# Optimization experiments

Hardware: AMD Instinct MI355X
Metric: run time of the kernel (lower is better)

Reference implementation:

```python
import jax, jax.numpy as jnp
import numpy as np

B, H, P, L = 8, 128, 128, 4096


def _cplx(x):
    # view_as_complex: (..., 2) float -> complex
    return x[..., 0] + 1j * x[..., 1]


def setup_inputs() -> dict:
    key = jax.random.key(0)
    ks = jax.random.split(key, 6)
    u = jax.random.normal(ks[0], (B, H, L), dtype=jnp.float32)
    C_ri = jax.random.normal(ks[1], (H, P, 2), dtype=jnp.float32)
    D_ri = jax.random.normal(ks[2], (H, H, 2), dtype=jnp.float32)
    # ContinuousStateReservoir: Re(Lambda) in [high_stability, low_stability] = [-1.0, -0.1]
    lam_re = jax.random.uniform(ks[3], (P,), minval=-1.0, maxval=-0.1, dtype=jnp.float32)
    lam_im = jax.random.normal(ks[4], (P,), dtype=jnp.float32) * np.float32(np.pi)
    Lam = lam_re + 1j * lam_im                      # continuous eigs
    Lam_bar = jnp.exp(Lam)                          # ZOH with Delta = 1
    B0 = jax.random.normal(ks[5], (P, H, 2), dtype=jnp.float32)
    Bc = _cplx(B0)
    B_bar = ((Lam_bar - 1.0) / Lam)[:, None] * Bc   # ZOH B_bar
    B_ri = jnp.stack([B_bar.real, B_bar.imag], axis=-1).astype(jnp.float32)
    Lambda_ri = jnp.stack([Lam_bar.real, Lam_bar.imag], axis=-1).astype(jnp.float32)
    return {"u": u, "C_ri": C_ri, "D_ri": D_ri, "B_ri": B_ri, "Lambda_ri": Lambda_ri}


def reference(u, C_ri, D_ri, B_ri, Lambda_ri):
    C = _cplx(C_ri)          # (H, P) complex
    D = _cplx(D_ri)          # (H, H)
    B_bar = _cplx(B_ri)      # (P, H)
    Lam_bar = _cplx(Lambda_ri)  # (P,)
    # torch.fft.rfftn defaults to ALL dims: complex FFT on (B,H), real FFT on L
    U_s = jnp.fft.rfftn(u)                                   # (B, H, Lf)
    s = 1j * (2.0 * jnp.pi * jnp.fft.rfftfreq(u.shape[-1]))  # (Lf,)
    mid = 1.0 / (s[None, :] - Lam_bar[:, None])              # (P, Lf) Cauchy kernel
    C_mid = jnp.einsum('hp,pl->hpl', C, mid)                 # (H, P, Lf)
    G = jnp.einsum('hpl,pq->hql', C_mid, B_bar)              # (H, H, Lf) transfer function
    Y_s = jnp.einsum('hql,bql->bhl', G, U_s) + jnp.einsum('hq,bql->bhl', D, U_s)
    y = jnp.fft.irfftn(Y_s)                                  # (B, H, L) real
    return jax.nn.gelu(y, approximate=False)
```

## Files before the change

kernel.cpp:

```cpp
#include <hip/hip_runtime.h>
#include <math.h>

#define Bn 8
#define Hn 128
#define Pn 128
#define Ln 4096
#define LF 2049
#define NROWS (Bn*Hn)
#define NT 32
#define NTILES 65
#define PLSZ 4096
#define WPLSZ 16384
#define TSCALE 64.0f

#define SKEW(a) ((a) + ((a) >> 4))
#define FBUF 2176

typedef _Float16 f16x8 __attribute__((ext_vector_type(8)));
typedef float f32x4 __attribute__((ext_vector_type(4)));

__device__ __forceinline__ void fsincos(float a, float* s, float* c) {
    *s = __sinf(a);
    *c = __cosf(a);
}

__device__ __forceinline__ void write2(_Float16* __restrict__ W, int idx,
                                       float vr, float vi) {
    W[0 * WPLSZ + idx] = (_Float16)vr;
    W[1 * WPLSZ + idx] = (_Float16)vi;
}

__global__ __launch_bounds__(256) void prep_all_k(
        const float* __restrict__ B_ri, const float* __restrict__ C_ri,
        const float* __restrict__ D_ri,
        _Float16* __restrict__ W1, _Float16* __restrict__ W2,
        _Float16* __restrict__ W3, float2* __restrict__ tw) {
    __shared__ float2 roots[128];
    __shared__ float2 stage[2048];
    __shared__ float2 Gs[8 * 128];
    const int bid = blockIdx.x;
    const int tid = threadIdx.x;

    if (tid < 128) {
        float ang = 3.14159265358979f * (float)tid / 64.0f;
        float sw, cw; fsincos(ang, &sw, &cw);
        roots[tid] = make_float2(cw, sw);
    }
    __syncthreads();

    if (bid < 64) {
        const float2* B2f = (const float2*)B_ri;
        stage[tid] = B2f[bid * 256 + tid];
        __syncthreads();
        const int pl = tid >> 7, h = tid & 127;
        float sr = 0.f, si = 0.f;
        #pragma unroll 8
        for (int q = 0; q < 128; ++q) {
            float2 rt = roots[(q * h) & 127];
            float2 bv = stage[(pl << 7) + q];
            sr += bv.x * rt.x + bv.y * rt.y;
            si += bv.y * rt.x - bv.x * rt.y;
        }
        write2(W1, bid * 256 + tid, sr, si);
    } else if (bid < 128) {
        const int bid2 = bid - 64;
        const float2* C2f = (const float2*)C_ri;
        const int h = 2 * bid2 + (tid >> 7), p = tid & 127;
        float sr = 0.f, si = 0.f;
        for (int chunk = 0; chunk < 8; ++chunk) {
            __syncthreads();
            #pragma unroll
            for (int i = 0; i < 8; ++i) stage[tid + i * 256] = C2f[chunk * 2048 + tid + i * 256];
            __syncthreads();
            #pragma unroll
            for (int j = 0; j < 16; ++j) {
                int h2 = chunk * 16 + j;
                float2 cv = stage[j * 128 + p];
                float2 rt = roots[(h * h2) & 127];
                sr += cv.x * rt.x - cv.y * rt.y;
                si += cv.x * rt.y + cv.y * rt.x;
            }
        }
        write2(W2, bid2 * 256 + tid, sr * (TSCALE / 128.0f), si * (TSCALE / 128.0f));
    } else if (bid < 144) {
        const int h0 = (bid - 128) * 8;
        const int hh = tid >> 5, ci = tid & 31;
        const float2* D2f = (const float2*)D_ri;
        float2 g[4];
        #pragma unroll
        for (int cc = 0; cc < 4; ++cc) g[cc] = make_float2(0.f, 0.f);
        for (int chunk = 0; chunk < 8; ++chunk) {
            __syncthreads();
            #pragma unroll
            for (int i = 0; i < 8; ++i) stage[tid + i * 256] = D2f[chunk * 2048 + tid + i * 256];
            __syncthreads();
            #pragma unroll
            for (int j = 0; j < 16; ++j) {
                int a = chunk * 16 + j;
                float2 rt = roots[((h0 + hh) * a) & 127];
                #pragma unroll
                for (int cc = 0; cc < 4; ++cc) {
                    float2 dv = stage[j * 128 + ci + 32 * cc];
                    g[cc].x += dv.x * rt.x - dv.y * rt.y;
                    g[cc].y += dv.x * rt.y + dv.y * rt.x;
                }
            }
        }
        #pragma unroll
        for (int cc = 0; cc < 4; ++cc)
            Gs[hh * 128 + ci + 32 * cc] = make_float2(g[cc].x * (1.0f / 128.0f),
                                                      g[cc].y * (1.0f / 128.0f));
        __syncthreads();
        float2 wacc[4];
        #pragma unroll
        for (int qq = 0; qq < 4; ++qq) wacc[qq] = make_float2(0.f, 0.f);
        #pragma unroll 4
        for (int c = 0; c < 128; ++c) {
            float2 gv = Gs[hh * 128 + c];
            #pragma unroll
            for (int qq = 0; qq < 4; ++qq) {
                int q = ci + 32 * qq;
                float2 rt = roots[(c * q) & 127];
                wacc[qq].x += gv.x * rt.x + gv.y * rt.y;
                wacc[qq].y += gv.y * rt.x - gv.x * rt.y;
            }
        }
        #pragma unroll
        for (int qq = 0; qq < 4; ++qq)
            write2(W3, (h0 + hh) * 128 + ci + 32 * qq, wacc[qq].x, wacc[qq].y);
    } else {
        int m = (bid - 144) * 256 + tid;
        float ang = -3.14159265358979f * (float)m / 1024.0f;
        float sw, cw;
        __sincosf(ang, &sw, &cw);
        tw[m] = make_float2(cw, sw);
    }
}

__device__ __forceinline__ float2 cadd2(float2 a, float2 b) { return make_float2(a.x + b.x, a.y + b.y); }
__device__ __forceinline__ float2 csub2(float2 a, float2 b) { return make_float2(a.x - b.x, a.y - b.y); }

template <int SIGN>
__device__ __forceinline__ void dft4(float2 a0, float2 a1, float2 a2, float2 a3,
                                     float2& y0, float2& y1, float2& y2, float2& y3) {
    float t0x = a0.x + a2.x, t0y = a0.y + a2.y;
    float t1x = a0.x - a2.x, t1y = a0.y - a2.y;
    float t2x = a1.x + a3.x, t2y = a1.y + a3.y;
    float t3x = a1.x - a3.x, t3y = a1.y - a3.y;
    y0 = make_float2(t0x + t2x, t0y + t2y);
    y2 = make_float2(t0x - t2x, t0y - t2y);
    y1 = make_float2(t1x - (float)SIGN * t3y, t1y + (float)SIGN * t3x);
    y3 = make_float2(t1x + (float)SIGN * t3y, t1y - (float)SIGN * t3x);
}

template <int SIGN>
__device__ __forceinline__ void fft2048(float2* bufA, float2* bufB,
                                        const float2* __restrict__ tw) {
    const int tid = threadIdx.x;
    float2* src = bufA;
    float2* dst = bufB;
    #pragma unroll
    for (int stg = 0; stg < 3; ++stg) {
        const int ls = 3 * stg;
        const int k = tid;
        const int q = k & ((1 << ls) - 1);
        const int mbase = k - q;
        float2 a[8];
        #pragma unroll
        for (int u = 0; u < 8; ++u) a[u] = src[SKEW(k + (u << 8))];
        float2 t1 = tw[mbase],     t2 = tw[2 * mbase], t3 = tw[3 * mbase];
        float2 t4 = tw[4 * mbase], t5 = tw[5 * mbase], t6 = tw[6 * mbase];
        float2 t7 = tw[7 * mbase];
        float2 A0, A1, A2, A3, B0, B1, B2, B3;
        dft4<SIGN>(a[0], a[2], a[4], a[6], A0, A1, A2, A3);
        dft4<SIGN>(a[1], a[3], a[5], a[7], B0, B1, B2, B3);
        const float c45 = 0.70710678118655f;
        float2 w1 = make_float2(c45 * (B1.x - (float)SIGN * B1.y), c45 * ((float)SIGN * B1.x + B1.y));
        float2 w2 = make_float2(-(float)SIGN * B2.y, (float)SIGN * B2.x);
        float2 w3 = make_float2(c45 * (-B3.x - (float)SIGN * B3.y), c45 * ((float)SIGN * B3.x - B3.y));
        float2 b[8];
        b[0] = cadd2(A0, B0);  b[4] = csub2(A0, B0);
        b[1] = cadd2(A1, w1);  b[5] = csub2(A1, w1);
        b[2] = cadd2(A2, w2);  b[6] = csub2(A2, w2);
        b[3] = cadd2(A3, w3);  b[7] = csub2(A3, w3);
        float2 twj[8];
        twj[1] = t1; twj[2] = t2; twj[3] = t3; twj[4] = t4;
        twj[5] = t5; twj[6] = t6; twj[7] = t7;
        #pragma unroll
        for (int j = 1; j < 8; ++j) {
            float cj = twj[j].x;
            float sj = (float)SIGN * twj[j].y;
            b[j] = make_float2(b[j].x * cj + b[j].y * sj, -b[j].x * sj + b[j].y * cj);
        }
        const int base = q + (mbase << 3);
        #pragma unroll
        for (int j = 0; j < 8; ++j) dst[SKEW(base + (j << ls))] = b[j];
        __syncthreads();
        float2* t = src; src = dst; dst = t;
    }
    #pragma unroll
    for (int r = 0; r < 2; ++r) {
        int k = tid + (r << 8);
        float2 a0 = src[SKEW(k)];
        float2 a1 = src[SKEW(k + 512)];
        float2 a2 = src[SKEW(k + 1024)];
        float2 a3 = src[SKEW(k + 1536)];
        float2 y0, y1, y2, y3;
        dft4<SIGN>(a0, a1, a2, a3, y0, y1, y2, y3);
        dst[SKEW(k)] = y0;
        dst[SKEW(k + 512)] = y1;
        dst[SKEW(k + 1024)] = y2;
        dst[SKEW(k + 1536)] = y3;
    }
    __syncthreads();
}

__global__ __launch_bounds__(256, 4) void rfft_rows_k(const float* __restrict__ u,
                                                      float2* __restrict__ Uhat,
                                                      const float2* __restrict__ tw) {
    __shared__ __align__(16) float2 bufA[FBUF];
    __shared__ __align__(16) float2 bufB[FBUF];
    const int row = blockIdx.x;
    const int tid = threadIdx.x;
    const float4* up4 = (const float4*)(u + (size_t)row * Ln);
    #pragma unroll
    for (int r = 0; r < 4; ++r) {
        float4 v = up4[tid + (r << 8)];
        int i = 2 * (tid + (r << 8));
        bufA[SKEW(i)] = make_float2(v.x, v.y);
        bufA[SKEW(i + 1)] = make_float2(v.z, v.w);
    }
    __syncthreads();
    fft2048<-1>(bufA, bufB, tw);
    float2* op = Uhat + (size_t)row * LF;
    for (int l = tid; l < 1025; l += 256) {
        float2 Zl = bufA[SKEW(l)];
        float2 Zm = bufA[SKEW((2048 - l) & 2047)];
        float2 Fe = make_float2(0.5f * (Zl.x + Zm.x), 0.5f * (Zl.y - Zm.y));
        float2 Dv = make_float2(0.5f * (Zl.x - Zm.x), 0.5f * (Zl.y + Zm.y));
        float2 Fo = make_float2(Dv.y, -Dv.x);
        float s, c; fsincos(-3.14159265358979f * (float)l / 2048.0f, &s, &c);
        float2 TF = make_float2(Fo.x * c - Fo.y * s, Fo.x * s + Fo.y * c);
        op[l] = make_float2(Fe.x + TF.x, Fe.y + TF.y);
        op[2048 - l] = make_float2(Fe.x - TF.x, -(Fe.y - TF.y));
    }
}

__global__ __launch_bounds__(256, 4) void irfft_gelu_k(const float2* __restrict__ Uhat,
                                                       float* __restrict__ out,
                                                       const float2* __restrict__ tw) {
    __shared__ __align__(16) float2 bufA[FBUF];
    __shared__ __align__(16) float2 bufB[FBUF];
    const int row = blockIdx.x;
    const int tid = threadIdx.x;
    const float2* wp = Uhat + (size_t)row * LF;
    for (int l = tid; l < 1025; l += 256) {
        float2 Ul = wp[l];
        float2 Um = wp[2048 - l];
        float2 Fe = make_float2(0.5f * (Ul.x + Um.x), 0.5f * (Ul.y - Um.y));
        float2 Dv = make_float2(0.5f * (Ul.x - Um.x), 0.5f * (Ul.y + Um.y));
        float s, c; fsincos(3.14159265358979f * (float)l / 2048.0f, &s, &c);
        float2 Fo = make_float2(Dv.x * c - Dv.y * s, Dv.x * s + Dv.y * c);
        bufA[SKEW(l)] = make_float2(Fe.x - Fo.y, Fe.y + Fo.x);
        if (l >= 1 && l <= 1023)
            bufA[SKEW(2048 - l)] = make_float2(Fe.x + Fo.y, Fo.x - Fe.y);
    }
    __syncthreads();
    fft2048<1>(bufA, bufB, tw);
    float4* op4 = (float4*)(out + (size_t)row * Ln);
    #pragma unroll
    for (int r = 0; r < 4; ++r) {
        int n = 2 * (tid + (r << 8));
        float2 z0 = bufA[SKEW(n)];
        float2 z1 = bufA[SKEW(n + 1)];
        float y0 = z0.x * (1.0f / 2048.0f);
        float y1 = z0.y * (1.0f / 2048.0f);
        float y2 = z1.x * (1.0f / 2048.0f);
        float y3 = z1.y * (1.0f / 2048.0f);
        op4[tid + (r << 8)] = make_float4(
            0.5f * y0 * (1.0f + erff(y0 * 0.70710678118655f)),
            0.5f * y1 * (1.0f + erff(y1 * 0.70710678118655f)),
            0.5f * y2 * (1.0f + erff(y2 * 0.70710678118655f)),
            0.5f * y3 * (1.0f + erff(y3 * 0.70710678118655f)));
    }
}

__device__ __forceinline__ f32x4 mfma16h(f16x8 a, f16x8 b, f32x4 c) {
    return __builtin_amdgcn_mfma_f32_16x16x32_f16(a, b, c, 0, 0, 0);
}
__device__ __forceinline__ f16x8 read_frag(const _Float16* plane, int n, int k) {
    int ksw = k ^ ((n & 7) << 3);
    return *(const f16x8*)(plane + n * 128 + ksw);
}
__device__ __forceinline__ f16x8 aread(const _Float16* W, int pl, int m, int k) {
    return *(const f16x8*)(W + pl * WPLSZ + m * 128 + k);
}

__global__ __launch_bounds__(256, 4) void mixmm_k(float2* __restrict__ Uhat,
                                                  const _Float16* __restrict__ W1,
                                                  const _Float16* __restrict__ W2,
                                                  const _Float16* __restrict__ W3,
                                                  const float* __restrict__ Lam) {
    __shared__ __align__(16) _Float16 Up[2 * PLSZ];
    __shared__ __align__(16) _Float16 Tp[2 * PLSZ];

    const int tid = threadIdx.x;
    const int b = blockIdx.x / NTILES;
    const int tile = blockIdx.x % NTILES;
    const int l0 = tile * NT;
    const int ncols = (LF - l0) < NT ? (LF - l0) : NT;

    {
        int n = tid & 31, kc = tid >> 5;
        float2 v[16];
        #pragma unroll
        for (int j = 0; j < 16; ++j) {
            int h = kc * 16 + j;
            v[j] = (n < ncols) ? Uhat[(size_t)(b * 128 + h) * LF + l0 + n]
                               : make_float2(0.f, 0.f);
        }
        #pragma unroll
        for (int jc = 0; jc < 2; ++jc) {
            f16x8 fr, fi;
            #pragma unroll
            for (int j = 0; j < 8; ++j) {
                fr[j] = (_Float16)v[jc * 8 + j].x;
                fi[j] = (_Float16)v[jc * 8 + j].y;
            }
            int ksw = (kc * 16 + jc * 8) ^ ((n & 7) << 3);
            *(f16x8*)(Up + 0 * PLSZ + n * 128 + ksw) = fr;
            *(f16x8*)(Up + 1 * PLSZ + n * 128 + ksw) = fi;
        }
    }
    __syncthreads();

    const int lane = tid & 63;
    const int w = tid >> 6;
    const int m15 = lane & 15;
    const int quad = lane >> 4;

    f32x4 accR[2][2], accM[2][2], accI[2][2];
    #pragma unroll
    for (int s = 0; s < 2; ++s)
        #pragma unroll
        for (int t = 0; t < 2; ++t) {
            accR[s][t] = (f32x4)0.f; accM[s][t] = (f32x4)0.f; accI[s][t] = (f32x4)0.f;
        }

    #pragma unroll
    for (int kb = 0; kb < 4; ++kb) {
        int k = kb * 32 + quad * 8;
        f16x8 wr[2], wi[2];
        #pragma unroll
        for (int s = 0; s < 2; ++s) {
            int m = w * 32 + s * 16 + m15;
            wr[s] = aread(W1, 0, m, k);
            wi[s] = aread(W1, 1, m, k);
        }
        f16x8 br[2], bi[2];
        #pragma unroll
        for (int t = 0; t < 2; ++t) {
            br[t] = read_frag(Up + 0 * PLSZ, t * 16 + m15, k);
            bi[t] = read_frag(Up + 1 * PLSZ, t * 16 + m15, k);
        }
        #pragma unroll
        for (int s = 0; s < 2; ++s)
            #pragma unroll
            for (int t = 0; t < 2; ++t) {
                accR[s][t] = mfma16h(wr[s], br[t], accR[s][t]);
                accM[s][t] = mfma16h(wi[s], bi[t], accM[s][t]);
                accI[s][t] = mfma16h(wr[s], bi[t], accI[s][t]);
                accI[s][t] = mfma16h(wi[s], br[t], accI[s][t]);
            }
    }

    #pragma unroll
    for (int s = 0; s < 2; ++s) {
        #pragma unroll
        for (int reg = 0; reg < 4; ++reg) {
            int p = w * 32 + s * 16 + quad * 4 + reg;
            float2 lamv = ((const float2*)Lam)[p];
            float dr = -lamv.x;
            #pragma unroll
            for (int t = 0; t < 2; ++t) {
                int n = t * 16 + m15;
                int l = l0 + n;
                float di = 3.14159265358979f * (float)l / 2048.0f - lamv.y;
                float inv = (1.0f / TSCALE) / (dr * dr + di * di);
                float xr = accR[s][t][reg] - accM[s][t][reg];
                float xi = accI[s][t][reg];
                float tr = (xr * dr + xi * di) * inv;
                float ti = (xi * dr - xr * di) * inv;
                int off = n * 128 + (p ^ ((n & 7) << 3));
                Tp[0 * PLSZ + off] = (_Float16)tr;
                Tp[1 * PLSZ + off] = (_Float16)ti;
            }
        }
    }
    __syncthreads();

    #pragma unroll
    for (int s = 0; s < 2; ++s)
        #pragma unroll
        for (int t = 0; t < 2; ++t) {
            accR[s][t] = (f32x4)0.f; accM[s][t] = (f32x4)0.f; accI[s][t] = (f32x4)0.f;
        }

    #pragma unroll
    for (int kb = 0; kb < 4; ++kb) {
        int k = kb * 32 + quad * 8;
        {
            f16x8 wr[2], wi[2];
            #pragma unroll
            for (int s = 0; s < 2; ++s) {
                int m = w * 32 + s * 16 + m15;
                wr[s] = aread(W2, 0, m, k);
                wi[s] = aread(W2, 1, m, k);
            }
            f16x8 br[2], bi[2];
            #pragma unroll
            for (int t = 0; t < 2; ++t) {
                br[t] = read_frag(Tp + 0 * PLSZ, t * 16 + m15, k);
                bi[t] = read_frag(Tp + 1 * PLSZ, t * 16 + m15, k);
            }
            #pragma unroll
            for (int s = 0; s < 2; ++s)
                #pragma unroll
                for (int t = 0; t < 2; ++t) {
                    accR[s][t] = mfma16h(wr[s], br[t], accR[s][t]);
                    accM[s][t] = mfma16h(wi[s], bi[t], accM[s][t]);
                    accI[s][t] = mfma16h(wr[s], bi[t], accI[s][t]);
                    accI[s][t] = mfma16h(wi[s], br[t], accI[s][t]);
                }
        }
        {
            f16x8 wr[2], wi[2];
            #pragma unroll
            for (int s = 0; s < 2; ++s) {
                int m = w * 32 + s * 16 + m15;
                wr[s] = aread(W3, 0, m, k);
                wi[s] = aread(W3, 1, m, k);
            }
            f16x8 br[2], bi[2];
            #pragma unroll
            for (int t = 0; t < 2; ++t) {
                br[t] = read_frag(Up + 0 * PLSZ, t * 16 + m15, k);
                bi[t] = read_frag(Up + 1 * PLSZ, t * 16 + m15, k);
            }
            #pragma unroll
            for (int s = 0; s < 2; ++s)
                #pragma unroll
                for (int t = 0; t < 2; ++t) {
                    accR[s][t] = mfma16h(wr[s], br[t], accR[s][t]);
                    accM[s][t] = mfma16h(wi[s], bi[t], accM[s][t]);
                    accI[s][t] = mfma16h(wr[s], bi[t], accI[s][t]);
                    accI[s][t] = mfma16h(wi[s], br[t], accI[s][t]);
                }
        }
    }

    #pragma unroll
    for (int s = 0; s < 2; ++s) {
        #pragma unroll
        for (int t = 0; t < 2; ++t) {
            int n = t * 16 + m15;
            if (n < ncols) {
                #pragma unroll
                for (int reg = 0; reg < 4; ++reg) {
                    int m = w * 32 + s * 16 + quad * 4 + reg;
                    Uhat[(size_t)(b * 128 + m) * LF + l0 + n] =
                        make_float2(accR[s][t][reg] - accM[s][t][reg], accI[s][t][reg]);
                }
            }
        }
    }
}

extern "C" void kernel_launch(void* const* d_in, const int* in_sizes, int n_in,
                              void* d_out, int out_size, void* d_ws, size_t ws_size,
                              hipStream_t stream) {
    const float* u    = (const float*)d_in[0];
    const float* C_ri = (const float*)d_in[1];
    const float* D_ri = (const float*)d_in[2];
    const float* B_ri = (const float*)d_in[3];
    const float* Lam  = (const float*)d_in[4];
    float* out = (float*)d_out;

    float2* Uhat = (float2*)d_ws;
    _Float16* W1 = (_Float16*)(Uhat + (size_t)NROWS * LF);
    _Float16* W2 = W1 + 2 * WPLSZ;
    _Float16* W3 = W2 + 2 * WPLSZ;
    float2* tw = (float2*)(W3 + 2 * WPLSZ);

    prep_all_k<<<152, 256, 0, stream>>>(B_ri, C_ri, D_ri, W1, W2, W3, tw);
    rfft_rows_k<<<NROWS, 256, 0, stream>>>(u, Uhat, tw);
    mixmm_k<<<Bn * NTILES, 256, 0, stream>>>(Uhat, W1, W2, W3, Lam);
    irfft_gelu_k<<<NROWS, 256, 0, stream>>>(Uhat, out, tw);
}
```

Measured before the change: 153.8 us.

## Replace radix-8 shared-memory FFT with four-step FFT using MFMA 128-point DFT

The 2048-point row FFTs in the forward and inverse kernels now use a 16x128 four-step decomposition. The radix-16 stage runs in registers, and the 128-point DFT stage runs as an fp16 MFMA matrix multiply against a precomputed DFT matrix. Each block now handles two rows, and the inverse FFT is done through conjugation. This moves FFT arithmetic onto the matrix cores and cuts the number of shared-memory passes and barriers. The cost is fp16 rounding of intermediate spectra, which adds accuracy risk, plus lower occupancy from launch bounds of 3 and larger shared memory.

```diff
diff --git a/kernel.cpp b/kernel.cpp
--- a/kernel.cpp
+++ b/kernel.cpp
@@ -3,7 +3,6 @@
 
 #define Bn 8
 #define Hn 128
-#define Pn 128
 #define Ln 4096
 #define LF 2049
 #define NROWS (Bn*Hn)
@@ -12,9 +11,12 @@
 #define PLSZ 4096
 #define WPLSZ 16384
 #define TSCALE 64.0f
+#define ISCALE 64.0f
 
 #define SKEW(a) ((a) + ((a) >> 4))
-#define FBUF 2176
+#define ZROW 2064
+#define XROW 2176
+#define ZIDX(n) (129 * ((n) >> 7) + ((n) & 127))
 
 typedef _Float16 f16x8 __attribute__((ext_vector_type(8)));
 typedef float f32x4 __attribute__((ext_vector_type(4)));
@@ -22,6 +24,22 @@
 __device__ __forceinline__ void fsincos(float a, float* s, float* c) {
     *s = __sinf(a);
     *c = __cosf(a);
+}
+__device__ __forceinline__ float2 cm(float2 a, float2 b) {
+    return make_float2(a.x * b.x - a.y * b.y, a.x * b.y + a.y * b.x);
+}
+
+template <int SIGN>
+__device__ __forceinline__ void dft4(float2 a0, float2 a1, float2 a2, float2 a3,
+                                     float2& y0, float2& y1, float2& y2, float2& y3) {
+    float t0x = a0.x + a2.x, t0y = a0.y + a2.y;
+    float t1x = a0.x - a2.x, t1y = a0.y - a2.y;
+    float t2x = a1.x + a3.x, t2y = a1.y + a3.y;
+    float t3x = a1.x - a3.x, t3y = a1.y - a3.y;
+    y0 = make_float2(t0x + t2x, t0y + t2y);
+    y2 = make_float2(t0x - t2x, t0y - t2y);
+    y1 = make_float2(t1x - (float)SIGN * t3y, t1y + (float)SIGN * t3x);
+    y3 = make_float2(t1x + (float)SIGN * t3y, t1y - (float)SIGN * t3x);
 }
 
 __device__ __forceinline__ void write2(_Float16* __restrict__ W, int idx,
@@ -34,7 +52,8 @@
         const float* __restrict__ B_ri, const float* __restrict__ C_ri,
         const float* __restrict__ D_ri,
         _Float16* __restrict__ W1, _Float16* __restrict__ W2,
-        _Float16* __restrict__ W3, float2* __restrict__ tw) {
+        _Float16* __restrict__ W3, float2* __restrict__ tw,
+        _Float16* __restrict__ F128) {
     __shared__ float2 roots[128];
     __shared__ float2 stage[2048];
     __shared__ float2 Gs[8 * 128];
@@ -128,160 +147,22 @@
         #pragma unroll
         for (int qq = 0; qq < 4; ++qq)
             write2(W3, (h0 + hh) * 128 + ci + 32 * qq, wacc[qq].x, wacc[qq].y);
-    } else {
+    } else if (bid < 152) {
         int m = (bid - 144) * 256 + tid;
         float ang = -3.14159265358979f * (float)m / 1024.0f;
         float sw, cw;
         __sincosf(ang, &sw, &cw);
         tw[m] = make_float2(cw, sw);
-    }
-}
-
-__device__ __forceinline__ float2 cadd2(float2 a, float2 b) { return make_float2(a.x + b.x, a.y + b.y); }
-__device__ __forceinline__ float2 csub2(float2 a, float2 b) { return make_float2(a.x - b.x, a.y - b.y); }
-
-template <int SIGN>
-__device__ __forceinline__ void dft4(float2 a0, float2 a1, float2 a2, float2 a3,
-                                     float2& y0, float2& y1, float2& y2, float2& y3) {
-    float t0x = a0.x + a2.x, t0y = a0.y + a2.y;
-    float t1x = a0.x - a2.x, t1y = a0.y - a2.y;
-    float t2x = a1.x + a3.x, t2y = a1.y + a3.y;
-    float t3x = a1.x - a3.x, t3y = a1.y - a3.y;
-    y0 = make_float2(t0x + t2x, t0y + t2y);
-    y2 = make_float2(t0x - t2x, t0y - t2y);
-    y1 = make_float2(t1x - (float)SIGN * t3y, t1y + (float)SIGN * t3x);
-    y3 = make_float2(t1x + (float)SIGN * t3y, t1y - (float)SIGN * t3x);
-}
-
-template <int SIGN>
-__device__ __forceinline__ void fft2048(float2* bufA, float2* bufB,
-                                        const float2* __restrict__ tw) {
-    const int tid = threadIdx.x;
-    float2* src = bufA;
-    float2* dst = bufB;
-    #pragma unroll
-    for (int stg = 0; stg < 3; ++stg) {
-        const int ls = 3 * stg;
-        const int k = tid;
-        const int q = k & ((1 << ls) - 1);
-        const int mbase = k - q;
-        float2 a[8];
-        #pragma unroll
-        for (int u = 0; u < 8; ++u) a[u] = src[SKEW(k + (u << 8))];
-        float2 t1 = tw[mbase],     t2 = tw[2 * mbase], t3 = tw[3 * mbase];
-        float2 t4 = tw[4 * mbase], t5 = tw[5 * mbase], t6 = tw[6 * mbase];
-        float2 t7 = tw[7 * mbase];
-        float2 A0, A1, A2, A3, B0, B1, B2, B3;
-        dft4<SIGN>(a[0], a[2], a[4], a[6], A0, A1, A2, A3);
-        dft4<SIGN>(a[1], a[3], a[5], a[7], B0, B1, B2, B3);
-        const float c45 = 0.70710678118655f;
-        float2 w1 = make_float2(c45 * (B1.x - (float)SIGN * B1.y), c45 * ((float)SIGN * B1.x + B1.y));
-        float2 w2 = make_float2(-(float)SIGN * B2.y, (float)SIGN * B2.x);
-        float2 w3 = make_float2(c45 * (-B3.x - (float)SIGN * B3.y), c45 * ((float)SIGN * B3.x - B3.y));
-        float2 b[8];
-        b[0] = cadd2(A0, B0);  b[4] = csub2(A0, B0);
-        b[1] = cadd2(A1, w1);  b[5] = csub2(A1, w1);
-        b[2] = cadd2(A2, w2);  b[6] = csub2(A2, w2);
-        b[3] = cadd2(A3, w3);  b[7] = csub2(A3, w3);
-        float2 twj[8];
-        twj[1] = t1; twj[2] = t2; twj[3] = t3; twj[4] = t4;
-        twj[5] = t5; twj[6] = t6; twj[7] = t7;
-        #pragma unroll
-        for (int j = 1; j < 8; ++j) {
-            float cj = twj[j].x;
-            float sj = (float)SIGN * twj[j].y;
-            b[j] = make_float2(b[j].x * cj + b[j].y * sj, -b[j].x * sj + b[j].y * cj);
-        }
-        const int base = q + (mbase << 3);
-        #pragma unroll
-        for (int j = 0; j < 8; ++j) dst[SKEW(base + (j << ls))] = b[j];
-        __syncthreads();
-        float2* t = src; src = dst; dst = t;
-    }
-    #pragma unroll
-    for (int r = 0; r < 2; ++r) {
-        int k = tid + (r << 8);
-        float2 a0 = src[SKEW(k)];
-        float2 a1 = src[SKEW(k + 512)];
-        float2 a2 = src[SKEW(k + 1024)];
-        float2 a3 = src[SKEW(k + 1536)];
-        float2 y0, y1, y2, y3;
-        dft4<SIGN>(a0, a1, a2, a3, y0, y1, y2, y3);
-        dst[SKEW(k)] = y0;
-        dst[SKEW(k + 512)] = y1;
-        dst[SKEW(k + 1024)] = y2;
-        dst[SKEW(k + 1536)] = y3;
-    }
-    __syncthreads();
-}
-
-__global__ __launch_bounds__(256, 4) void rfft_rows_k(const float* __restrict__ u,
-                                                      float2* __restrict__ Uhat,
-                                                      const float2* __restrict__ tw) {
-    __shared__ __align__(16) float2 bufA[FBUF];
-    __shared__ __align__(16) float2 bufB[FBUF];
-    const int row = blockIdx.x;
-    const int tid = threadIdx.x;
-    const float4* up4 = (const float4*)(u + (size_t)row * Ln);
-    #pragma unroll
-    for (int r = 0; r < 4; ++r) {
-        float4 v = up4[tid + (r << 8)];
-        int i = 2 * (tid + (r << 8));
-        bufA[SKEW(i)] = make_float2(v.x, v.y);
-        bufA[SKEW(i + 1)] = make_float2(v.z, v.w);
-    }
-    __syncthreads();
-    fft2048<-1>(bufA, bufB, tw);
-    float2* op = Uhat + (size_t)row * LF;
-    for (int l = tid; l < 1025; l += 256) {
-        float2 Zl = bufA[SKEW(l)];
-        float2 Zm = bufA[SKEW((2048 - l) & 2047)];
-        float2 Fe = make_float2(0.5f * (Zl.x + Zm.x), 0.5f * (Zl.y - Zm.y));
-        float2 Dv = make_float2(0.5f * (Zl.x - Zm.x), 0.5f * (Zl.y + Zm.y));
-        float2 Fo = make_float2(Dv.y, -Dv.x);
-        float s, c; fsincos(-3.14159265358979f * (float)l / 2048.0f, &s, &c);
-        float2 TF = make_float2(Fo.x * c - Fo.y * s, Fo.x * s + Fo.y * c);
-        op[l] = make_float2(Fe.x + TF.x, Fe.y + TF.y);
-        op[2048 - l] = make_float2(Fe.x - TF.x, -(Fe.y - TF.y));
-    }
-}
-
-__global__ __launch_bounds__(256, 4) void irfft_gelu_k(const float2* __restrict__ Uhat,
-                                                       float* __restrict__ out,
-                                                       const float2* __restrict__ tw) {
-    __shared__ __align__(16) float2 bufA[FBUF];
-    __shared__ __align__(16) float2 bufB[FBUF];
-    const int row = blockIdx.x;
-    const int tid = threadIdx.x;
-    const float2* wp = Uhat + (size_t)row * LF;
-    for (int l = tid; l < 1025; l += 256) {
-        float2 Ul = wp[l];
-        float2 Um = wp[2048 - l];
-        float2 Fe = make_float2(0.5f * (Ul.x + Um.x), 0.5f * (Ul.y - Um.y));
-        float2 Dv = make_float2(0.5f * (Ul.x - Um.x), 0.5f * (Ul.y + Um.y));
-        float s, c; fsincos(3.14159265358979f * (float)l / 2048.0f, &s, &c);
-        float2 Fo = make_float2(Dv.x * c - Dv.y * s, Dv.x * s + Dv.y * c);
-        bufA[SKEW(l)] = make_float2(Fe.x - Fo.y, Fe.y + Fo.x);
-        if (l >= 1 && l <= 1023)
-            bufA[SKEW(2048 - l)] = make_float2(Fe.x + Fo.y, Fo.x - Fe.y);
-    }
-    __syncthreads();
-    fft2048<1>(bufA, bufB, tw);
-    float4* op4 = (float4*)(out + (size_t)row * Ln);
-    #pragma unroll
-    for (int r = 0; r < 4; ++r) {
-        int n = 2 * (tid + (r << 8));
-        float2 z0 = bufA[SKEW(n)];
-        float2 z1 = bufA[SKEW(n + 1)];
-        float y0 = z0.x * (1.0f / 2048.0f);
-        float y1 = z0.y * (1.0f / 2048.0f);
-        float y2 = z1.x * (1.0f / 2048.0f);
-        float y3 = z1.y * (1.0f / 2048.0f);
-        op4[tid + (r << 8)] = make_float4(
-            0.5f * y0 * (1.0f + erff(y0 * 0.70710678118655f)),
-            0.5f * y1 * (1.0f + erff(y1 * 0.70710678118655f)),
-            0.5f * y2 * (1.0f + erff(y2 * 0.70710678118655f)),
-            0.5f * y3 * (1.0f + erff(y3 * 0.70710678118655f)));
+    } else {
+        #pragma unroll
+        for (int j = 0; j < 8; ++j) {
+            int e = (bid - 152) * 2048 + tid + j * 256;
+            int m = e >> 7, k = e & 127;
+            float ang = -3.14159265358979f * (float)((m * k) & 127) / 64.0f;
+            float sw, cw; fsincos(ang, &sw, &cw);
+            F128[e] = (_Float16)cw;
+            F128[WPLSZ + e] = (_Float16)sw;
+        }
     }
 }
 
@@ -294,6 +175,185 @@
 }
 __device__ __forceinline__ f16x8 aread(const _Float16* W, int pl, int m, int k) {
     return *(const f16x8*)(W + pl * WPLSZ + m * 128 + k);
+}
+
+__device__ __forceinline__ void fourstep2048(float2* zx, _Float16* Bpl,
+                                             const _Float16* __restrict__ F128,
+                                             const float2* __restrict__ tw,
+                                             int tid, float bscale) {
+    {
+        const int rl = tid >> 7, n1 = tid & 127;
+        float2 a[16];
+        #pragma unroll
+        for (int n2 = 0; n2 < 16; ++n2) a[n2] = zx[rl * ZROW + 129 * n2 + n1];
+        const float2 K1 = make_float2(0.92387953f, -0.38268343f);
+        const float2 K2 = make_float2(0.70710678f, -0.70710678f);
+        const float2 K3 = make_float2(0.38268343f, -0.92387953f);
+        const float2 K4 = make_float2(0.f, -1.f);
+        const float2 K6 = make_float2(-0.70710678f, -0.70710678f);
+        const float2 K9 = make_float2(-0.92387953f, 0.38268343f);
+        float2 b16[16], y0, y1, y2, y3;
+        dft4<-1>(a[0], a[4], a[8], a[12], y0, y1, y2, y3);
+        b16[0] = y0; b16[1] = y1; b16[2] = y2; b16[3] = y3;
+        dft4<-1>(a[1], a[5], a[9], a[13], y0, y1, y2, y3);
+        b16[4] = y0; b16[5] = cm(y1, K1); b16[6] = cm(y2, K2); b16[7] = cm(y3, K3);
+        dft4<-1>(a[2], a[6], a[10], a[14], y0, y1, y2, y3);
+        b16[8] = y0; b16[9] = cm(y1, K2); b16[10] = cm(y2, K4); b16[11] = cm(y3, K6);
+        dft4<-1>(a[3], a[7], a[11], a[15], y0, y1, y2, y3);
+        b16[12] = y0; b16[13] = cm(y1, K3); b16[14] = cm(y2, K6); b16[15] = cm(y3, K9);
+        float2 X16[16];
+        #pragma unroll
+        for (int q = 0; q < 4; ++q) {
+            dft4<-1>(b16[q], b16[q + 4], b16[q + 8], b16[q + 12], y0, y1, y2, y3);
+            X16[q] = y0; X16[q + 4] = y1; X16[q + 8] = y2; X16[q + 12] = y3;
+        }
+        #pragma unroll
+        for (int k2 = 0; k2 < 16; ++k2) {
+            float2 v = X16[k2];
+            if (k2) v = cm(v, tw[(n1 * k2) & 2047]);
+            int n = rl * 16 + k2;
+            int ksw = n1 ^ ((n & 7) << 3);
+            Bpl[0 * PLSZ + n * 128 + ksw] = (_Float16)(v.x * bscale);
+            Bpl[1 * PLSZ + n * 128 + ksw] = (_Float16)(v.y * bscale);
+        }
+    }
+    __syncthreads();
+
+    const int lane = tid & 63;
+    const int w = tid >> 6;
+    const int m15 = lane & 15;
+    const int quad = lane >> 4;
+    f32x4 accR[2][2], accM[2][2], accI[2][2];
+    #pragma unroll
+    for (int s = 0; s < 2; ++s)
+        #pragma unroll
+        for (int t = 0; t < 2; ++t) {
+            accR[s][t] = (f32x4)0.f; accM[s][t] = (f32x4)0.f; accI[s][t] = (f32x4)0.f;
+        }
+    #pragma unroll
+    for (int kb = 0; kb < 4; ++kb) {
+        int k = kb * 32 + quad * 8;
+        f16x8 wr[2], wi[2];
+        #pragma unroll
+        for (int s = 0; s < 2; ++s) {
+            int m = w * 32 + s * 16 + m15;
+            wr[s] = aread(F128, 0, m, k);
+            wi[s] = aread(F128, 1, m, k);
+        }
+        f16x8 br[2], bi[2];
+        #pragma unroll
+        for (int t = 0; t < 2; ++t) {
+            br[t] = read_frag(Bpl + 0 * PLSZ, t * 16 + m15, k);
+            bi[t] = read_frag(Bpl + 1 * PLSZ, t * 16 + m15, k);
+        }
+        #pragma unroll
+        for (int s = 0; s < 2; ++s)
+            #pragma unroll
+            for (int t = 0; t < 2; ++t) {
+                accR[s][t] = mfma16h(wr[s], br[t], accR[s][t]);
+                accM[s][t] = mfma16h(wi[s], bi[t], accM[s][t]);
+                accI[s][t] = mfma16h(wr[s], bi[t], accI[s][t]);
+                accI[s][t] = mfma16h(wi[s], br[t], accI[s][t]);
+            }
+    }
+    #pragma unroll
+    for (int s = 0; s < 2; ++s)
+        #pragma unroll
+        for (int t = 0; t < 2; ++t)
+            #pragma unroll
+            for (int reg = 0; reg < 4; ++reg) {
+                int k1 = w * 32 + s * 16 + quad * 4 + reg;
+                zx[t * XROW + SKEW(m15 + 16 * k1)] =
+                    make_float2(accR[s][t][reg] - accM[s][t][reg], accI[s][t][reg]);
+            }
+    __syncthreads();
+}
+
+__global__ __launch_bounds__(256, 3) void rfft_rows_k(const float* __restrict__ u,
+                                                      float2* __restrict__ Uhat,
+                                                      const float2* __restrict__ tw,
+                                                      const _Float16* __restrict__ F128) {
+    __shared__ __align__(16) float2 zx[2 * XROW];
+    __shared__ __align__(16) _Float16 Bpl[2 * PLSZ];
+    const int tid = threadIdx.x;
+    const int row0 = 2 * blockIdx.x;
+    const float4* up4 = (const float4*)(u + (size_t)row0 * Ln);
+    #pragma unroll
+    for (int r = 0; r < 8; ++r) {
+        int g = tid + (r << 8);
+        float4 v = up4[g];
+        int rl = g >> 10, f = g & 1023;
+        int n = 2 * f;
+        int dst = rl * ZROW + 129 * (n >> 7) + (n & 127);
+        zx[dst] = make_float2(v.x, v.y);
+        zx[dst + 1] = make_float2(v.z, v.w);
+    }
+    __syncthreads();
+    fourstep2048(zx, Bpl, F128, tw, tid, 1.0f);
+    #pragma unroll
+    for (int r = 0; r < 2; ++r) {
+        float2* op = Uhat + (size_t)(row0 + r) * LF;
+        const float2* X = zx + r * XROW;
+        for (int l = tid; l < 1025; l += 256) {
+            float2 Zl = X[SKEW(l)];
+            float2 Zm = X[SKEW((2048 - l) & 2047)];
+            float2 Fe = make_float2(0.5f * (Zl.x + Zm.x), 0.5f * (Zl.y - Zm.y));
+            float2 Dv = make_float2(0.5f * (Zl.x - Zm.x), 0.5f * (Zl.y + Zm.y));
+            float2 Fo = make_float2(Dv.y, -Dv.x);
+            float s, c; fsincos(-3.14159265358979f * (float)l / 2048.0f, &s, &c);
+            float2 TF = make_float2(Fo.x * c - Fo.y * s, Fo.x * s + Fo.y * c);
+            op[l] = make_float2(Fe.x + TF.x, Fe.y + TF.y);
+            op[2048 - l] = make_float2(Fe.x - TF.x, -(Fe.y - TF.y));
+        }
+    }
+}
+
+__global__ __launch_bounds__(256, 3) void irfft_gelu_k(const float2* __restrict__ Uhat,
+                                                       float* __restrict__ out,
+                                                       const float2* __restrict__ tw,
+                                                       const _Float16* __restrict__ F128) {
+    __shared__ __align__(16) float2 zx[2 * XROW];
+    __shared__ __align__(16) _Float16 Bpl[2 * PLSZ];
+    const int tid = threadIdx.x;
+    const int row0 = 2 * blockIdx.x;
+    #pragma unroll
+    for (int r = 0; r < 2; ++r) {
+        const float2* wp = Uhat + (size_t)(row0 + r) * LF;
+        float2* zr = zx + r * ZROW;
+        for (int l = tid; l < 1025; l += 256) {
+            float2 Ul = wp[l];
+            float2 Um = wp[2048 - l];
+            float2 Fe = make_float2(0.5f * (Ul.x + Um.x), 0.5f * (Ul.y - Um.y));
+            float2 Dv = make_float2(0.5f * (Ul.x - Um.x), 0.5f * (Ul.y + Um.y));
+            float s, c; fsincos(3.14159265358979f * (float)l / 2048.0f, &s, &c);
+            float2 Fo = make_float2(Dv.x * c - Dv.y * s, Dv.x * s + Dv.y * c);
+            zr[ZIDX(l)] = make_float2(Fe.x - Fo.y, -(Fe.y + Fo.x));
+            if (l >= 1 && l <= 1023)
+                zr[ZIDX(2048 - l)] = make_float2(Fe.x + Fo.y, Fe.y - Fo.x);
+        }
+    }
+    __syncthreads();
+    fourstep2048(zx, Bpl, F128, tw, tid, 1.0f / ISCALE);
+    const float SC = ISCALE / 2048.0f;
+    #pragma unroll
+    for (int r = 0; r < 2; ++r) {
+        float4* op4 = (float4*)(out + (size_t)(row0 + r) * Ln);
+        const float2* X = zx + r * XROW;
+        #pragma unroll
+        for (int rr = 0; rr < 4; ++rr) {
+            int i = tid + (rr << 8);
+            int n = 2 * i;
+            float2 z0 = X[SKEW(n)];
+            float2 z1 = X[SKEW(n + 1)];
+            float y0 = z0.x * SC, y1 = -z0.y * SC;
+            float y2 = z1.x * SC, y3 = -z1.y * SC;
+            op4[i] = make_float4(
+                0.5f * y0 * (1.0f + erff(y0 * 0.70710678118655f)),
+                0.5f * y1 * (1.0f + erff(y1 * 0.70710678118655f)),
+                0.5f * y2 * (1.0f + erff(y2 * 0.70710678118655f)),
+                0.5f * y3 * (1.0f + erff(y3 * 0.70710678118655f)));
+        }
+    }
 }
 
 __global__ __launch_bounds__(256, 4) void mixmm_k(float2* __restrict__ Uhat,
@@ -491,9 +551,10 @@
     _Float16* W2 = W1 + 2 * WPLSZ;
     _Float16* W3 = W2 + 2 * WPLSZ;
     float2* tw = (float2*)(W3 + 2 * WPLSZ);
-
-    prep_all_k<<<152, 256, 0, stream>>>(B_ri, C_ri, D_ri, W1, W2, W3, tw);
-    rfft_rows_k<<<NROWS, 256, 0, stream>>>(u, Uhat, tw);
+    _Float16* F128 = (_Float16*)(tw + 2048);
+
+    prep_all_k<<<160, 256, 0, stream>>>(B_ri, C_ri, D_ri, W1, W2, W3, tw, F128);
+    rfft_rows_k<<<NROWS / 2, 256, 0, stream>>>(u, Uhat, tw, F128);
     mixmm_k<<<Bn * NTILES, 256, 0, stream>>>(Uhat, W1, W2, W3, Lam);
-    irfft_gelu_k<<<NROWS, 256, 0, stream>>>(Uhat, out, tw);
-}
+    irfft_gelu_k<<<NROWS / 2, 256, 0, stream>>>(Uhat, out, tw, F128);
+}
```

Measured after the change: 159.7 us. +3.8%, slower.

## Fuse rfft, mixing GEMM and irfft+GELU into one persistent kernel with grid barriers

Applied to the files above, without the earlier changes.

Replaces the three launches for forward FFT, spectral mixing and inverse FFT with GELU by a single 512-block persistent kernel. Each block handles two rows per FFT phase and one or two mixing tiles, and phases are separated by atomic-counter grid barriers whose counters are reset in the prep kernel. Shared memory is aliased between the FFT buffers and the GEMM tiles. The aim is to remove launch gaps and tail effects between kernels. In exchange it relies on all 512 blocks being co-resident (launch bounds of 3 blocks per CU), adds spin-wait cost, and leaves the mixing phase load-imbalanced since 8 blocks do an extra tile.

```diff
diff --git a/kernel.cpp b/kernel.cpp
--- a/kernel.cpp
+++ b/kernel.cpp
@@ -3,12 +3,12 @@
 
 #define Bn 8
 #define Hn 128
-#define Pn 128
 #define Ln 4096
 #define LF 2049
 #define NROWS (Bn*Hn)
 #define NT 32
 #define NTILES 65
+#define NBLK 512
 #define PLSZ 4096
 #define WPLSZ 16384
 #define TSCALE 64.0f
@@ -34,7 +34,8 @@
         const float* __restrict__ B_ri, const float* __restrict__ C_ri,
         const float* __restrict__ D_ri,
         _Float16* __restrict__ W1, _Float16* __restrict__ W2,
-        _Float16* __restrict__ W3, float2* __restrict__ tw) {
+        _Float16* __restrict__ W3, float2* __restrict__ tw,
+        unsigned int* __restrict__ bar) {
     __shared__ float2 roots[128];
     __shared__ float2 stage[2048];
     __shared__ float2 Gs[8 * 128];
@@ -134,7 +135,18 @@
         float sw, cw;
         __sincosf(ang, &sw, &cw);
         tw[m] = make_float2(cw, sw);
-    }
+        if (bid == 144 && tid < 2) bar[tid] = 0u;
+    }
+}
+
+__device__ __forceinline__ void grid_barrier(unsigned int* cnt, unsigned int target) {
+    __syncthreads();
+    if (threadIdx.x == 0) {
+        __hip_atomic_fetch_add(cnt, 1u, __ATOMIC_ACQ_REL, __HIP_MEMORY_SCOPE_AGENT);
+        while (__hip_atomic_load(cnt, __ATOMIC_ACQUIRE, __HIP_MEMORY_SCOPE_AGENT) < target)
+            __builtin_amdgcn_s_sleep(8);
+    }
+    __syncthreads();
 }
 
 __device__ __forceinline__ float2 cadd2(float2 a, float2 b) { return make_float2(a.x + b.x, a.y + b.y); }
@@ -215,76 +227,6 @@
     __syncthreads();
 }
 
-__global__ __launch_bounds__(256, 4) void rfft_rows_k(const float* __restrict__ u,
-                                                      float2* __restrict__ Uhat,
-                                                      const float2* __restrict__ tw) {
-    __shared__ __align__(16) float2 bufA[FBUF];
-    __shared__ __align__(16) float2 bufB[FBUF];
-    const int row = blockIdx.x;
-    const int tid = threadIdx.x;
-    const float4* up4 = (const float4*)(u + (size_t)row * Ln);
-    #pragma unroll
-    for (int r = 0; r < 4; ++r) {
-        float4 v = up4[tid + (r << 8)];
-        int i = 2 * (tid + (r << 8));
-        bufA[SKEW(i)] = make_float2(v.x, v.y);
-        bufA[SKEW(i + 1)] = make_float2(v.z, v.w);
-    }
-    __syncthreads();
-    fft2048<-1>(bufA, bufB, tw);
-    float2* op = Uhat + (size_t)row * LF;
-    for (int l = tid; l < 1025; l += 256) {
-        float2 Zl = bufA[SKEW(l)];
-        float2 Zm = bufA[SKEW((2048 - l) & 2047)];
-        float2 Fe = make_float2(0.5f * (Zl.x + Zm.x), 0.5f * (Zl.y - Zm.y));
-        float2 Dv = make_float2(0.5f * (Zl.x - Zm.x), 0.5f * (Zl.y + Zm.y));
-        float2 Fo = make_float2(Dv.y, -Dv.x);
-        float s, c; fsincos(-3.14159265358979f * (float)l / 2048.0f, &s, &c);
-        float2 TF = make_float2(Fo.x * c - Fo.y * s, Fo.x * s + Fo.y * c);
-        op[l] = make_float2(Fe.x + TF.x, Fe.y + TF.y);
-        op[2048 - l] = make_float2(Fe.x - TF.x, -(Fe.y - TF.y));
-    }
-}
-
-__global__ __launch_bounds__(256, 4) void irfft_gelu_k(const float2* __restrict__ Uhat,
-                                                       float* __restrict__ out,
-                                                       const float2* __restrict__ tw) {
-    __shared__ __align__(16) float2 bufA[FBUF];
-    __shared__ __align__(16) float2 bufB[FBUF];
-    const int row = blockIdx.x;
-    const int tid = threadIdx.x;
-    const float2* wp = Uhat + (size_t)row * LF;
-    for (int l = tid; l < 1025; l += 256) {
-        float2 Ul = wp[l];
-        float2 Um = wp[2048 - l];
-        float2 Fe = make_float2(0.5f * (Ul.x + Um.x), 0.5f * (Ul.y - Um.y));
-        float2 Dv = make_float2(0.5f * (Ul.x - Um.x), 0.5f * (Ul.y + Um.y));
-        float s, c; fsincos(3.14159265358979f * (float)l / 2048.0f, &s, &c);
-        float2 Fo = make_float2(Dv.x * c - Dv.y * s, Dv.x * s + Dv.y * c);
-        bufA[SKEW(l)] = make_float2(Fe.x - Fo.y, Fe.y + Fo.x);
-        if (l >= 1 && l <= 1023)
-            bufA[SKEW(2048 - l)] = make_float2(Fe.x + Fo.y, Fo.x - Fe.y);
-    }
-    __syncthreads();
-    fft2048<1>(bufA, bufB, tw);
-    float4* op4 = (float4*)(out + (size_t)row * Ln);
-    #pragma unroll
-    for (int r = 0; r < 4; ++r) {
-        int n = 2 * (tid + (r << 8));
-        float2 z0 = bufA[SKEW(n)];
-        float2 z1 = bufA[SKEW(n + 1)];
-        float y0 = z0.x * (1.0f / 2048.0f);
-        float y1 = z0.y * (1.0f / 2048.0f);
-        float y2 = z1.x * (1.0f / 2048.0f);
-        float y3 = z1.y * (1.0f / 2048.0f);
-        op4[tid + (r << 8)] = make_float4(
-            0.5f * y0 * (1.0f + erff(y0 * 0.70710678118655f)),
-            0.5f * y1 * (1.0f + erff(y1 * 0.70710678118655f)),
-            0.5f * y2 * (1.0f + erff(y2 * 0.70710678118655f)),
-            0.5f * y3 * (1.0f + erff(y3 * 0.70710678118655f)));
-    }
-}
-
 __device__ __forceinline__ f32x4 mfma16h(f16x8 a, f16x8 b, f32x4 c) {
     return __builtin_amdgcn_mfma_f32_16x16x32_f16(a, b, c, 0, 0, 0);
 }
@@ -296,17 +238,12 @@
     return *(const f16x8*)(W + pl * WPLSZ + m * 128 + k);
 }
 
-__global__ __launch_bounds__(256, 4) void mixmm_k(float2* __restrict__ Uhat,
-                                                  const _Float16* __restrict__ W1,
-                                                  const _Float16* __restrict__ W2,
-                                                  const _Float16* __restrict__ W3,
-                                                  const float* __restrict__ Lam) {
-    __shared__ __align__(16) _Float16 Up[2 * PLSZ];
-    __shared__ __align__(16) _Float16 Tp[2 * PLSZ];
-
-    const int tid = threadIdx.x;
-    const int b = blockIdx.x / NTILES;
-    const int tile = blockIdx.x % NTILES;
+__device__ void mix_tile(int g, float2* __restrict__ Uhat,
+                         const _Float16* __restrict__ W1, const _Float16* __restrict__ W2,
+                         const _Float16* __restrict__ W3, const float* __restrict__ Lam,
+                         _Float16* Up, _Float16* Tp, int tid) {
+    const int b = g / NTILES;
+    const int tile = g % NTILES;
     const int l0 = tile * NT;
     const int ncols = (LF - l0) < NT ? (LF - l0) : NT;
 
@@ -476,6 +413,94 @@
     }
 }
 
+__global__ __launch_bounds__(256, 3) void fused_k(
+        const float* __restrict__ u, float* __restrict__ out,
+        float2* __restrict__ Uhat,
+        const _Float16* __restrict__ W1, const _Float16* __restrict__ W2,
+        const _Float16* __restrict__ W3, const float* __restrict__ Lam,
+        const float2* __restrict__ tw, unsigned int* __restrict__ bar) {
+    __shared__ __align__(16) unsigned char smem[2 * FBUF * sizeof(float2)];
+    float2* bufA = (float2*)smem;
+    float2* bufB = bufA + FBUF;
+    _Float16* Up = (_Float16*)smem;
+    _Float16* Tp = Up + 2 * PLSZ;
+
+    const int tid = threadIdx.x;
+    const int bid = blockIdx.x;
+
+    #pragma unroll 1
+    for (int r = 0; r < 2; ++r) {
+        const int row = 2 * bid + r;
+        const float4* up4 = (const float4*)(u + (size_t)row * Ln);
+        #pragma unroll
+        for (int rr = 0; rr < 4; ++rr) {
+            float4 v = up4[tid + (rr << 8)];
+            int i = 2 * (tid + (rr << 8));
+            bufA[SKEW(i)] = make_float2(v.x, v.y);
+            bufA[SKEW(i + 1)] = make_float2(v.z, v.w);
+        }
+        __syncthreads();
+        fft2048<-1>(bufA, bufB, tw);
+        float2* op = Uhat + (size_t)row * LF;
+        for (int l = tid; l < 1025; l += 256) {
+            float2 Zl = bufA[SKEW(l)];
+            float2 Zm = bufA[SKEW((2048 - l) & 2047)];
+            float2 Fe = make_float2(0.5f * (Zl.x + Zm.x), 0.5f * (Zl.y - Zm.y));
+            float2 Dv = make_float2(0.5f * (Zl.x - Zm.x), 0.5f * (Zl.y + Zm.y));
+            float2 Fo = make_float2(Dv.y, -Dv.x);
+            float s, c; fsincos(-3.14159265358979f * (float)l / 2048.0f, &s, &c);
+            float2 TF = make_float2(Fo.x * c - Fo.y * s, Fo.x * s + Fo.y * c);
+            op[l] = make_float2(Fe.x + TF.x, Fe.y + TF.y);
+            op[2048 - l] = make_float2(Fe.x - TF.x, -(Fe.y - TF.y));
+        }
+        __syncthreads();
+    }
+    grid_barrier(&bar[0], NBLK);
+
+    mix_tile(bid, Uhat, W1, W2, W3, Lam, Up, Tp, tid);
+    if (bid < 8) {
+        __syncthreads();
+        mix_tile(NBLK + bid, Uhat, W1, W2, W3, Lam, Up, Tp, tid);
+    }
+    grid_barrier(&bar[1], NBLK);
+
+    #pragma unroll 1
+    for (int r = 0; r < 2; ++r) {
+        const int row = 2 * bid + r;
+        const float2* wp = Uhat + (size_t)row * LF;
+        for (int l = tid; l < 1025; l += 256) {
+            float2 Ul = wp[l];
+            float2 Um = wp[2048 - l];
+            float2 Fe = make_float2(0.5f * (Ul.x + Um.x), 0.5f * (Ul.y - Um.y));
+            float2 Dv = make_float2(0.5f * (Ul.x - Um.x), 0.5f * (Ul.y + Um.y));
+            float s, c; fsincos(3.14159265358979f * (float)l / 2048.0f, &s, &c);
+            float2 Fo = make_float2(Dv.x * c - Dv.y * s, Dv.x * s + Dv.y * c);
+            bufA[SKEW(l)] = make_float2(Fe.x - Fo.y, Fe.y + Fo.x);
+            if (l >= 1 && l <= 1023)
+                bufA[SKEW(2048 - l)] = make_float2(Fe.x + Fo.y, Fo.x - Fe.y);
+        }
+        __syncthreads();
+        fft2048<1>(bufA, bufB, tw);
+        float4* op4 = (float4*)(out + (size_t)row * Ln);
+        #pragma unroll
+        for (int rr = 0; rr < 4; ++rr) {
+            int n = 2 * (tid + (rr << 8));
+            float2 z0 = bufA[SKEW(n)];
+            float2 z1 = bufA[SKEW(n + 1)];
+            float y0 = z0.x * (1.0f / 2048.0f);
+            float y1 = z0.y * (1.0f / 2048.0f);
+            float y2 = z1.x * (1.0f / 2048.0f);
+            float y3 = z1.y * (1.0f / 2048.0f);
+            op4[tid + (rr << 8)] = make_float4(
+                0.5f * y0 * (1.0f + erff(y0 * 0.70710678118655f)),
+                0.5f * y1 * (1.0f + erff(y1 * 0.70710678118655f)),
+                0.5f * y2 * (1.0f + erff(y2 * 0.70710678118655f)),
+                0.5f * y3 * (1.0f + erff(y3 * 0.70710678118655f)));
+        }
+        __syncthreads();
+    }
+}
+
 extern "C" void kernel_launch(void* const* d_in, const int* in_sizes, int n_in,
                               void* d_out, int out_size, void* d_ws, size_t ws_size,
                               hipStream_t stream) {
@@ -491,9 +516,8 @@
     _Float16* W2 = W1 + 2 * WPLSZ;
     _Float16* W3 = W2 + 2 * WPLSZ;
     float2* tw = (float2*)(W3 + 2 * WPLSZ);
-
-    prep_all_k<<<152, 256, 0, stream>>>(B_ri, C_ri, D_ri, W1, W2, W3, tw);
-    rfft_rows_k<<<NROWS, 256, 0, stream>>>(u, Uhat, tw);
-    mixmm_k<<<Bn * NTILES, 256, 0, stream>>>(Uhat, W1, W2, W3, Lam);
-    irfft_gelu_k<<<NROWS, 256, 0, stream>>>(Uhat, out, tw);
-}
+    unsigned int* bar = (unsigned int*)(tw + 2048);
+
+    prep_all_k<<<152, 256, 0, stream>>>(B_ri, C_ri, D_ri, W1, W2, W3, tw, bar);
+    fused_k<<<NBLK, 256, 0, stream>>>(u, out, Uhat, W1, W2, W3, Lam, tw, bar);
+}
```

New measurement: 367.2 us. 139% more time.
